# Optimization experiments

Hardware: AMD Instinct MI355X
Metric: run time of the kernel (lower is better)

The kernel has to match this reference:

```python
import jax, jax.numpy as jnp
import numpy as np
from jax import lax

B, D, DEPTH, H, P, NP, IMG, PS = 16, 384, 6, 6, 2000, 4, 224, 16
N = (IMG // PS) ** 2  # 196 patches
T = N + 1             # +cls token
TEMP = 100.0
NEG = -100000.0


def layernorm(x, s, b, eps=1e-6):
    m = jnp.mean(x, -1, keepdims=True)
    v = jnp.var(x, -1, keepdims=True)
    return (x - m) * lax.rsqrt(v + eps) * s + b


def setup_inputs() -> dict:
    key = jax.random.key(0)
    ks = jax.random.split(key, 16)
    s = 0.02
    inp = {
        "x": jax.random.normal(ks[0], (B, 3, IMG, IMG), jnp.float32),
        "patch_w": jax.random.normal(ks[1], (D, 3, PS, PS), jnp.float32) * s,
        "patch_b": jnp.zeros((D,), jnp.float32),
        "cls_token": jax.random.normal(ks[2], (1, 1, D), jnp.float32) * s,
        "pos_embed": jax.random.normal(ks[3], (1, T, D), jnp.float32) * s,
        "ln1_s": jnp.ones((DEPTH, D), jnp.float32),
        "ln1_b": jnp.zeros((DEPTH, D), jnp.float32),
        "qkv_w": jax.random.normal(ks[4], (DEPTH, D, 3 * D), jnp.float32) * s,
        "qkv_b": jnp.zeros((DEPTH, 3 * D), jnp.float32),
        "proj_w": jax.random.normal(ks[5], (DEPTH, D, D), jnp.float32) * s,
        "proj_b": jnp.zeros((DEPTH, D), jnp.float32),
        "ln2_s": jnp.ones((DEPTH, D), jnp.float32),
        "ln2_b": jnp.zeros((DEPTH, D), jnp.float32),
        "fc1_w": jax.random.normal(ks[6], (DEPTH, D, 4 * D), jnp.float32) * s,
        "fc1_b": jnp.zeros((DEPTH, 4 * D), jnp.float32),
        "fc2_w": jax.random.normal(ks[7], (DEPTH, 4 * D, D), jnp.float32) * s,
        "fc2_b": jnp.zeros((DEPTH, D), jnp.float32),
        "norm_s": jnp.ones((D,), jnp.float32),
        "norm_b": jnp.zeros((D,), jnp.float32),
        "proto": jax.random.normal(ks[8], (P, D, NP), jnp.float32),
        "patch_select": jnp.full((1, P, NP), 0.1, jnp.float32),
    }
    return inp


def vit_features(x, patch_w, patch_b, cls_token, pos_embed, blk, norm_s, norm_b):
    # patch embed: non-overlapping 16x16 conv, NCHW/OIHW
    f = lax.conv_general_dilated(x, patch_w, (PS, PS), "VALID",
                                 dimension_numbers=("NCHW", "OIHW", "NCHW"))
    f = f + patch_b[None, :, None, None]              # (B, D, 14, 14)
    tok = f.reshape(B, D, N).transpose(0, 2, 1)        # (B, N, D)
    tok = jnp.concatenate([jnp.broadcast_to(cls_token, (B, 1, D)), tok], axis=1)
    tok = tok + pos_embed

    hd = D // H
    scale = hd ** -0.5

    def block(t, p):
        l1s, l1b, qw, qb, pw, pb, l2s, l2b, f1w, f1b, f2w, f2b = p
        h = layernorm(t, l1s, l1b)
        qkv = h @ qw + qb                              # (B, T, 3D)
        q, k, v = jnp.split(qkv, 3, axis=-1)
        q = q.reshape(B, T, H, hd).transpose(0, 2, 1, 3)
        k = k.reshape(B, T, H, hd).transpose(0, 2, 1, 3)
        v = v.reshape(B, T, H, hd).transpose(0, 2, 1, 3)
        att = jax.nn.softmax(jnp.einsum("bhqd,bhkd->bhqk", q, k) * scale, axis=-1)
        o = jnp.einsum("bhqk,bhkd->bhqd", att, v).transpose(0, 2, 1, 3).reshape(B, T, D)
        t = t + (o @ pw + pb)
        h = layernorm(t, l2s, l2b)
        t = t + (jax.nn.gelu(h @ f1w + f1b, approximate=False) @ f2w + f2b)
        return t, None

    tok, _ = lax.scan(block, tok, blk)
    tok = layernorm(tok, norm_s, norm_b)
    cls = tok[:, 0]                                    # (B, D)
    x_focal = tok[:, 1:] - cls[:, None, :]             # (B, N, D)
    feat = x_focal.transpose(0, 2, 1)                  # (B, D, N) == (B,D,14,14) flat
    return feat, cls


def reference(x, patch_w, patch_b, cls_token, pos_embed, ln1_s, ln1_b, qkv_w,
              qkv_b, proj_w, proj_b, ln2_s, ln2_b, fc1_w, fc1_b, fc2_w, fc2_b,
              norm_s, norm_b, proto, patch_select):
    blk = (ln1_s, ln1_b, qkv_w, qkv_b, proj_w, proj_b, ln2_s, ln2_b,
           fc1_w, fc1_b, fc2_w, fc2_b)
    feat, cls = vit_features(x, patch_w, patch_b, cls_token, pos_embed, blk,
                             norm_s, norm_b)
    # L2-normalize over channel dim (torch F.normalize, eps=1e-12)
    fn = feat / jnp.maximum(jnp.linalg.norm(feat, axis=1, keepdims=True), 1e-12)
    pn = proto / jnp.maximum(jnp.linalg.norm(proto, axis=1, keepdims=True), 1e-12)
    # cosine sims for every (prototype, patch, subpatch): (B, P, N, NP)
    dist = jnp.einsum("bdn,pdk->bpnk", fn, pn).reshape(B, P, N * NP)

    slots = jax.nn.sigmoid(patch_select * TEMP)        # (1, P, NP)
    factor = slots.sum(-1, keepdims=True) + 1e-10

    mask = jnp.ones((B, P, N * NP), dist.dtype)
    col = jnp.arange(N * NP)
    vals = []
    for _ in range(NP):  # greedy non-overlapping subpatch matching
        dm = dist + (1.0 - mask) * NEG
        ids = jnp.argmax(dm, axis=-1)                  # (B, P)
        vals.append(jnp.take_along_axis(dm, ids[..., None], axis=-1)[..., 0])
        mask = jnp.where(col[None, None, :] == ids[..., None], 0.0, mask)
    values = jnp.stack(vals, axis=-1)                  # (B, P, NP)
    proto_scores = (values * (slots * NP / factor)).sum(-1)  # (B, P)
    return cls, proto_scores
```

## Files before the change

### kernel.cpp

```cpp
#include <hip/hip_runtime.h>
#include <hip/hip_bf16.h>
#include <math.h>


#define MROWS 3152

typedef short bf16x8 __attribute__((ext_vector_type(8)));
typedef float f32x4 __attribute__((ext_vector_type(4)));
typedef unsigned short u16;

__device__ __forceinline__ void async_copy16(void* lds, const void* g) {
    __builtin_amdgcn_global_load_lds((const __attribute__((address_space(1))) unsigned int*)g,
                                     (__attribute__((address_space(3))) unsigned int*)lds,
                                     16, 0, 0);
}

__device__ __forceinline__ u16 f2b(float x) {
    __hip_bfloat16 h = __float2bfloat16(x);
    return *(u16*)&h;
}

__global__ void k_cvt(const float* __restrict__ in, __hip_bfloat16* __restrict__ o, int n) {
    int i = blockIdx.x * 256 + threadIdx.x;
    if (i < n) o[i] = __float2bfloat16(in[i]);
}

__global__ __launch_bounds__(256) void k_wt(const float* __restrict__ W, __hip_bfloat16* __restrict__ Wt,
                                            int K, int N) {
    __shared__ float t[32][33];
    const float* src = W + (size_t)blockIdx.z * K * N;
    __hip_bfloat16* dst = Wt + (size_t)blockIdx.z * K * N;
    int n0 = blockIdx.x * 32, k0 = blockIdx.y * 32;
    int tx = threadIdx.x & 31, ty = threadIdx.x >> 5;
    #pragma unroll
    for (int i = 0; i < 4; ++i) t[ty + i * 8][tx] = src[(size_t)(k0 + ty + i * 8) * N + n0 + tx];
    __syncthreads();
    #pragma unroll
    for (int i = 0; i < 4; ++i)
        dst[(size_t)(n0 + ty + i * 8) * K + k0 + tx] = __float2bfloat16(t[tx][ty + i * 8]);
}

__global__ void k_im2col(const float* __restrict__ x, __hip_bfloat16* __restrict__ Acol) {
    int idx = blockIdx.x * 256 + threadIdx.x;
    int k = idx % 768;
    int m = idx / 768;
    int b = m / 196, n = m % 196;
    int c = k >> 8, rem = k & 255, i = rem >> 4, j = rem & 15;
    int py = n / 14, px = n % 14;
    Acol[idx] = __float2bfloat16(x[((b * 3 + c) * 224 + py * 16 + i) * 224 + px * 16 + j]);
}

template<int RES, int GELU, int BF16OUT>
__global__ __launch_bounds__(256) void k_mfma_gemm(
    const u16* __restrict__ A, const u16* __restrict__ Bt,
    const float* __restrict__ bias, const float* __restrict__ res,
    float* __restrict__ Cf, __hip_bfloat16* __restrict__ Cb,
    int M, int N, int K)
{
    __shared__ u16 As[2][128 * 64];
    __shared__ u16 Bs[2][128 * 64];
    const int tid = threadIdx.x;
    const int wid = tid >> 6, lane = tid & 63;
    const int m0 = blockIdx.y * 128, n0 = blockIdx.x * 128;
    const int srow = tid >> 3;
    const int selem = (tid & 7) << 3;
    const int wm = (wid >> 1) * 64, wn = (wid & 1) * 64;

    f32x4 acc[4][4] = {};

    auto stage = [&](int buf, int kb) {
        #pragma unroll
        for (int g = 0; g < 4; ++g) {
            int r = g * 32 + srow;
            int sw = selem ^ ((r & 7) << 3);
            int gr = m0 + r; if (gr > M - 1) gr = M - 1;
            async_copy16(&As[buf][r * 64 + selem], A + (size_t)gr * K + kb + sw);
            async_copy16(&Bs[buf][r * 64 + selem], Bt + (size_t)(n0 + r) * K + kb + sw);
        }
    };

    const int nk = K >> 6;
    stage(0, 0);
    __syncthreads();
    for (int t = 0; t < nk; ++t) {
        const int cur = t & 1;
        if (t + 1 < nk) stage(cur ^ 1, (t + 1) << 6);
        #pragma unroll
        for (int ks = 0; ks < 64; ks += 32) {
            const int kk = ks + ((lane >> 4) << 3);
            bf16x8 af[4], bfr[4];
            #pragma unroll
            for (int i = 0; i < 4; ++i) {
                int r = wm + i * 16 + (lane & 15);
                af[i] = *(const bf16x8*)&As[cur][r * 64 + (kk ^ ((r & 7) << 3))];
            }
            #pragma unroll
            for (int j = 0; j < 4; ++j) {
                int r = wn + j * 16 + (lane & 15);
                bfr[j] = *(const bf16x8*)&Bs[cur][r * 64 + (kk ^ ((r & 7) << 3))];
            }
            #pragma unroll
            for (int i = 0; i < 4; ++i)
                #pragma unroll
                for (int j = 0; j < 4; ++j)
                    acc[i][j] = __builtin_amdgcn_mfma_f32_16x16x32_bf16(af[i], bfr[j], acc[i][j], 0, 0, 0);
        }
        __syncthreads();
    }
    const int cl = lane & 15, rg = (lane >> 4) << 2;
    #pragma unroll
    for (int i = 0; i < 4; ++i) {
        #pragma unroll
        for (int j = 0; j < 4; ++j) {
            const int col = n0 + wn + j * 16 + cl;
            const float bv = bias[col];
            #pragma unroll
            for (int r = 0; r < 4; ++r) {
                const int row = m0 + wm + i * 16 + rg + r;
                if (row >= M) continue;
                float v = acc[i][j][r] + bv;
                if (RES) v += res[(size_t)row * N + col];
                if (GELU) v = 0.5f * v * (1.0f + erff(v * 0.70710678118f));
                if (BF16OUT) Cb[(size_t)row * N + col] = __float2bfloat16(v);
                else         Cf[(size_t)row * N + col] = v;
            }
        }
    }
}

template<int RES, int GELU, int BF16OUT>
__global__ __launch_bounds__(256) void k_mfma_gemm64(
    const u16* __restrict__ A, const u16* __restrict__ Bt,
    const float* __restrict__ bias, const float* __restrict__ res,
    float* __restrict__ Cf, __hip_bfloat16* __restrict__ Cb,
    int M, int N, int K)
{
    __shared__ u16 As[2][128 * 64];
    __shared__ u16 Bs[2][64 * 64];
    const int tid = threadIdx.x;
    const int wid = tid >> 6, lane = tid & 63;
    const int m0 = blockIdx.y * 128, n0 = blockIdx.x * 64;
    const int srow = tid >> 3;
    const int selem = (tid & 7) << 3;
    const int wm = wid * 32;

    f32x4 acc[2][4] = {};

    auto stage = [&](int buf, int kb) {
        #pragma unroll
        for (int g = 0; g < 4; ++g) {
            int r = g * 32 + srow;
            int sw = selem ^ ((r & 7) << 3);
            int gr = m0 + r; if (gr > M - 1) gr = M - 1;
            async_copy16(&As[buf][r * 64 + selem], A + (size_t)gr * K + kb + sw);
        }
        #pragma unroll
        for (int g = 0; g < 2; ++g) {
            int r = g * 32 + srow;
            int sw = selem ^ ((r & 7) << 3);
            async_copy16(&Bs[buf][r * 64 + selem], Bt + (size_t)(n0 + r) * K + kb + sw);
        }
    };

    const int nk = K >> 6;
    stage(0, 0);
    __syncthreads();
    for (int t = 0; t < nk; ++t) {
        const int cur = t & 1;
        if (t + 1 < nk) stage(cur ^ 1, (t + 1) << 6);
        #pragma unroll
        for (int ks = 0; ks < 64; ks += 32) {
            const int kk = ks + ((lane >> 4) << 3);
            bf16x8 af[2], bfr[4];
            #pragma unroll
            for (int i = 0; i < 2; ++i) {
                int r = wm + i * 16 + (lane & 15);
                af[i] = *(const bf16x8*)&As[cur][r * 64 + (kk ^ ((r & 7) << 3))];
            }
            #pragma unroll
            for (int j = 0; j < 4; ++j) {
                int r = j * 16 + (lane & 15);
                bfr[j] = *(const bf16x8*)&Bs[cur][r * 64 + (kk ^ ((r & 7) << 3))];
            }
            #pragma unroll
            for (int i = 0; i < 2; ++i)
                #pragma unroll
                for (int j = 0; j < 4; ++j)
                    acc[i][j] = __builtin_amdgcn_mfma_f32_16x16x32_bf16(af[i], bfr[j], acc[i][j], 0, 0, 0);
        }
        __syncthreads();
    }
    const int cl = lane & 15, rg = (lane >> 4) << 2;
    #pragma unroll
    for (int i = 0; i < 2; ++i) {
        #pragma unroll
        for (int j = 0; j < 4; ++j) {
            const int col = n0 + j * 16 + cl;
            const float bv = bias[col];
            #pragma unroll
            for (int r = 0; r < 4; ++r) {
                const int row = m0 + wm + i * 16 + rg + r;
                if (row >= M) continue;
                float v = acc[i][j][r] + bv;
                if (RES) v += res[(size_t)row * N + col];
                if (GELU) v = 0.5f * v * (1.0f + erff(v * 0.70710678118f));
                if (BF16OUT) Cb[(size_t)row * N + col] = __float2bfloat16(v);
                else         Cf[(size_t)row * N + col] = v;
            }
        }
    }
}

__global__ void k_assemble(const float* __restrict__ ptmp, const float* __restrict__ cls_tok,
                           const float* __restrict__ pos, float* __restrict__ tok) {
    int idx = blockIdx.x * 256 + threadIdx.x;
    int d = idx % 384;
    int t = (idx / 384) % 197;
    int b = idx / (384 * 197);
    float v = (t == 0) ? cls_tok[d] : ptmp[((size_t)b * 196 + t - 1) * 384 + d];
    tok[idx] = v + pos[t * 384 + d];
}

template<typename OT>
__global__ __launch_bounds__(256) void k_ln(const float* __restrict__ X, const float* __restrict__ s,
                                            const float* __restrict__ bb, OT* __restrict__ Y, int rows) {
    int wid = threadIdx.x >> 6, lane = threadIdx.x & 63;
    int row = blockIdx.x * 4 + wid;
    if (row >= rows) return;
    const float* x = X + (size_t)row * 384;
    float v[6], sum = 0.f, sq = 0.f;
    #pragma unroll
    for (int i = 0; i < 6; ++i) { float t = x[lane + 64 * i]; v[i] = t; sum += t; sq += t * t; }
    #pragma unroll
    for (int m = 32; m > 0; m >>= 1) { sum += __shfl_xor(sum, m); sq += __shfl_xor(sq, m); }
    float mean = sum * (1.f / 384.f);
    float var  = sq * (1.f / 384.f) - mean * mean;
    float rstd = rsqrtf(var + 1e-6f);
    OT* y = Y + (size_t)row * 384;
    #pragma unroll
    for (int i = 0; i < 6; ++i) {
        int d = lane + 64 * i;
        float o = (v[i] - mean) * rstd * s[d] + bb[d];
        y[d] = (OT)o;
    }
}

__global__ __launch_bounds__(256) void k_attn_mfma(const u16* __restrict__ qkv, u16* __restrict__ o) {
    __shared__ u16 Ks[208 * 64];
    __shared__ u16 VT[64 * 256];
    __shared__ u16 Pl[4][16 * 256];
    const int bh = blockIdx.x;
    const int b = bh / 6, hh = bh % 6;
    const u16* base = qkv + (size_t)b * 197 * 1152 + hh * 64;
    const int tid = threadIdx.x, wid = tid >> 6, lane = tid & 63;

    for (int i = tid; i < 64 * 59; i += 256) {
        int d = i / 59, k = 197 + i % 59;
        VT[d * 256 + (k ^ ((d & 7) << 3))] = 0;
    }
    for (int i = tid; i < 64 * 48; i += 256) {
        int q = i / 48, k = 208 + i % 48;
        Pl[q >> 4][(q & 15) * 256 + (k ^ ((q & 7) << 3))] = 0;
    }
    for (int i = tid; i < 197 * 8; i += 256) {
        int r = i >> 3, cc = (i & 7) << 3;
        uint4 v = *(const uint4*)(base + (size_t)r * 1152 + 384 + cc);
        *(uint4*)&Ks[r * 64 + (cc ^ ((r & 7) << 3))] = v;
    }
    for (int i = tid; i < 197 * 8; i += 256) {
        int r = i >> 3, d0 = (i & 7) << 3;
        uint4 v = *(const uint4*)(base + (size_t)r * 1152 + 768 + d0);
        const u16* pv = (const u16*)&v;
        #pragma unroll
        for (int j = 0; j < 8; ++j) {
            int d = d0 + j;
            VT[d * 256 + (r ^ ((d & 7) << 3))] = pv[j];
        }
    }
    __syncthreads();

    const int g = lane >> 4, c = lane & 15;
    const int t0 = blockIdx.y * 7;
    const int nt = blockIdx.y ? 6 : 7;
    for (int t = wid; t < nt; t += 4) {
        const int qt = t0 + t;
        const int q0 = qt * 16;
        int qrow = q0 + c; if (qrow > 196) qrow = 196;
        bf16x8 aq[2];
        aq[0] = *(const bf16x8*)(base + (size_t)qrow * 1152 + g * 8);
        aq[1] = *(const bf16x8*)(base + (size_t)qrow * 1152 + 32 + g * 8);

        f32x4 acc[13] = {};
        #pragma unroll
        for (int j = 0; j < 13; ++j) {
            int kr = j * 16 + c;
            bf16x8 b0 = *(const bf16x8*)&Ks[kr * 64 + ((g * 8) ^ ((kr & 7) << 3))];
            bf16x8 b1 = *(const bf16x8*)&Ks[kr * 64 + ((32 + g * 8) ^ ((kr & 7) << 3))];
            acc[j] = __builtin_amdgcn_mfma_f32_16x16x32_bf16(aq[0], b0, acc[j], 0, 0, 0);
            acc[j] = __builtin_amdgcn_mfma_f32_16x16x32_bf16(aq[1], b1, acc[j], 0, 0, 0);
        }

        float sc[13][4];
        float mr[4] = {-1e30f, -1e30f, -1e30f, -1e30f};
        #pragma unroll
        for (int j = 0; j < 13; ++j) {
            bool valid = (j * 16 + c) < 197;
            #pragma unroll
            for (int r = 0; r < 4; ++r) {
                float v = valid ? acc[j][r] * 0.125f : -1e30f;
                sc[j][r] = v;
                mr[r] = fmaxf(mr[r], v);
            }
        }
        #pragma unroll
        for (int r = 0; r < 4; ++r) {
            #pragma unroll
            for (int msk = 1; msk <= 8; msk <<= 1) mr[r] = fmaxf(mr[r], __shfl_xor(mr[r], msk));
        }
        float lr[4] = {0.f, 0.f, 0.f, 0.f};
        #pragma unroll
        for (int j = 0; j < 13; ++j)
            #pragma unroll
            for (int r = 0; r < 4; ++r) { float e = __expf(sc[j][r] - mr[r]); sc[j][r] = e; lr[r] += e; }
        #pragma unroll
        for (int r = 0; r < 4; ++r) {
            #pragma unroll
            for (int msk = 1; msk <= 8; msk <<= 1) lr[r] += __shfl_xor(lr[r], msk);
            lr[r] = 1.f / lr[r];
        }
        #pragma unroll
        for (int j = 0; j < 13; ++j) {
            int col = j * 16 + c;
            #pragma unroll
            for (int r = 0; r < 4; ++r) {
                int q = g * 4 + r;
                Pl[wid][q * 256 + (col ^ ((q & 7) << 3))] = f2b(sc[j][r] * lr[r]);
            }
        }
        asm volatile("s_waitcnt lgkmcnt(0)" ::: "memory");

        f32x4 av[4] = {};
        #pragma unroll
        for (int ks = 0; ks < 7; ++ks) {
            int kk = ks * 32 + g * 8;
            bf16x8 ap = *(const bf16x8*)&Pl[wid][c * 256 + (kk ^ ((c & 7) << 3))];
            #pragma unroll
            for (int jd = 0; jd < 4; ++jd) {
                int dr = jd * 16 + c;
                bf16x8 bv = *(const bf16x8*)&VT[dr * 256 + (kk ^ ((dr & 7) << 3))];
                av[jd] = __builtin_amdgcn_mfma_f32_16x16x32_bf16(ap, bv, av[jd], 0, 0, 0);
            }
        }
        #pragma unroll
        for (int jd = 0; jd < 4; ++jd) {
            #pragma unroll
            for (int r = 0; r < 4; ++r) {
                int q = q0 + g * 4 + r;
                if (q < 197)
                    o[((size_t)b * 197 + q) * 384 + hh * 64 + jd * 16 + c] = f2b(av[jd][r]);
            }
        }
    }
}

__global__ __launch_bounds__(256) void k_fn(const float* __restrict__ tokn, __hip_bfloat16* __restrict__ fn,
                                            float* __restrict__ out) {
    int wid = threadIdx.x >> 6, lane = threadIdx.x & 63;
    int row = blockIdx.x * 4 + wid;
    int b = row / 196, n = row % 196;
    const float* xr = tokn + ((size_t)b * 197 + 1 + n) * 384;
    const float* cr = tokn + (size_t)b * 197 * 384;
    float v[6], ss = 0.f;
    #pragma unroll
    for (int i = 0; i < 6; ++i) {
        int d = lane + 64 * i;
        float t = xr[d] - cr[d];
        v[i] = t; ss += t * t;
    }
    #pragma unroll
    for (int m = 32; m > 0; m >>= 1) ss += __shfl_xor(ss, m);
    float inv = 1.f / fmaxf(sqrtf(ss), 1e-12f);
    #pragma unroll
    for (int i = 0; i < 6; ++i) fn[(size_t)row * 384 + lane + 64 * i] = __float2bfloat16(v[i] * inv);
    int idx = blockIdx.x * 256 + threadIdx.x;
    if (idx < 6144) out[idx] = tokn[(size_t)(idx / 384) * 197 * 384 + idx % 384];
}

__global__ __launch_bounds__(256) void k_pn(const float* __restrict__ proto, __hip_bfloat16* __restrict__ pn) {
    int p = blockIdx.x;
    int k = threadIdx.x >> 6, lane = threadIdx.x & 63;
    float v[6], ss = 0.f;
    #pragma unroll
    for (int i = 0; i < 6; ++i) {
        int d = lane + 64 * i;
        float t = proto[((size_t)p * 384 + d) * 4 + k];
        v[i] = t; ss += t * t;
    }
    #pragma unroll
    for (int m = 32; m > 0; m >>= 1) ss += __shfl_xor(ss, m);
    float inv = 1.f / fmaxf(sqrtf(ss), 1e-12f);
    #pragma unroll
    for (int i = 0; i < 6; ++i) pn[((size_t)p * 4 + k) * 384 + lane + 64 * i] = __float2bfloat16(v[i] * inv);
}

__device__ __forceinline__ void top4_insert(float v, float& t0, float& t1, float& t2, float& t3) {
    if (v > t3) {
        t3 = v;
        if (t3 > t2) { float t = t2; t2 = t3; t3 = t; }
        if (t2 > t1) { float t = t1; t1 = t2; t2 = t; }
        if (t1 > t0) { float t = t0; t0 = t1; t1 = t; }
    }
}

__global__ __launch_bounds__(256) void k_dist_mfma(
    const __hip_bfloat16* __restrict__ fnb, const __hip_bfloat16* __restrict__ pnb,
    const float* __restrict__ psel, float* __restrict__ out)
{
    __shared__ u16 Ap[128 * 64];
    __shared__ u16 Bf[208 * 64];
    const u16* fn = (const u16*)fnb;
    const u16* pn = (const u16*)pnb;
    const int b = blockIdx.x;
    const int pb = blockIdx.y;
    const int tid = threadIdx.x, wid = tid >> 6, lane = tid & 63;
    const int srow = tid >> 3;
    const int selem = (tid & 7) << 3;

    f32x4 acc[2][13] = {};

    for (int kt = 0; kt < 384; kt += 64) {
        __syncthreads();
        #pragma unroll
        for (int g = 0; g < 4; ++g) {
            int r = g * 32 + srow;
            int gr = pb * 128 + r; if (gr > 7999) gr = 7999;
            async_copy16(&Ap[r * 64 + selem],
                         pn + (size_t)gr * 384 + kt + (selem ^ ((r & 7) << 3)));
        }
        #pragma unroll
        for (int g = 0; g < 7; ++g) {
            int r = g * 32 + srow;
            if (r < 208) {
                int fr = r > 195 ? 195 : r;
                async_copy16(&Bf[r * 64 + selem],
                             fn + ((size_t)b * 196 + fr) * 384 + kt + (selem ^ ((r & 7) << 3)));
            }
        }
        __syncthreads();
        #pragma unroll
        for (int ks = 0; ks < 64; ks += 32) {
            const int kk = ks + ((lane >> 4) << 3);
            bf16x8 af[2];
            #pragma unroll
            for (int i = 0; i < 2; ++i) {
                int r = wid * 32 + i * 16 + (lane & 15);
                af[i] = *(const bf16x8*)&Ap[r * 64 + (kk ^ ((r & 7) << 3))];
            }
            #pragma unroll
            for (int j = 0; j < 13; ++j) {
                int r = j * 16 + (lane & 15);
                bf16x8 bj = *(const bf16x8*)&Bf[r * 64 + (kk ^ ((r & 7) << 3))];
                acc[0][j] = __builtin_amdgcn_mfma_f32_16x16x32_bf16(af[0], bj, acc[0][j], 0, 0, 0);
                acc[1][j] = __builtin_amdgcn_mfma_f32_16x16x32_bf16(af[1], bj, acc[1][j], 0, 0, 0);
            }
        }
    }
    const int cl = lane & 15;
    #pragma unroll
    for (int mi = 0; mi < 2; ++mi) {
        float t0 = -1e30f, t1 = -1e30f, t2 = -1e30f, t3 = -1e30f;
        #pragma unroll
        for (int j = 0; j < 13; ++j) {
            if (j * 16 + cl >= 196) continue;
            #pragma unroll
            for (int r = 0; r < 4; ++r) top4_insert(acc[mi][j][r], t0, t1, t2, t3);
        }
        #pragma unroll
        for (int m = 1; m <= 8; m <<= 1) {
            float u0 = __shfl_xor(t0, m), u1 = __shfl_xor(t1, m);
            float u2 = __shfl_xor(t2, m), u3 = __shfl_xor(t3, m);
            top4_insert(u0, t0, t1, t2, t3);
            top4_insert(u1, t0, t1, t2, t3);
            top4_insert(u2, t0, t1, t2, t3);
            top4_insert(u3, t0, t1, t2, t3);
        }
        if (cl == 0) {
            int proto = pb * 32 + wid * 8 + mi * 4 + (lane >> 4);
            if (proto < 2000) {
                float sl[4], fac = 1e-10f;
                #pragma unroll
                for (int i = 0; i < 4; ++i) {
                    sl[i] = 1.f / (1.f + expf(-psel[proto * 4 + i] * 100.f));
                    fac += sl[i];
                }
                float score = (t0 * sl[0] + t1 * sl[1] + t2 * sl[2] + t3 * sl[3]) * 4.f / fac;
                out[6144 + (size_t)b * 2000 + proto] = score;
            }
        }
    }
}

extern "C" void kernel_launch(void* const* d_in, const int* in_sizes, int n_in,
                              void* d_out, int out_size, void* d_ws, size_t ws_size,
                              hipStream_t stream) {
    const float* x       = (const float*)d_in[0];
    const float* patch_w = (const float*)d_in[1];
    const float* patch_b = (const float*)d_in[2];
    const float* cls_tok = (const float*)d_in[3];
    const float* pos     = (const float*)d_in[4];
    const float* ln1_s   = (const float*)d_in[5];
    const float* ln1_b   = (const float*)d_in[6];
    const float* qkv_w   = (const float*)d_in[7];
    const float* qkv_b   = (const float*)d_in[8];
    const float* proj_w  = (const float*)d_in[9];
    const float* proj_b  = (const float*)d_in[10];
    const float* ln2_s   = (const float*)d_in[11];
    const float* ln2_b   = (const float*)d_in[12];
    const float* fc1_w   = (const float*)d_in[13];
    const float* fc1_b   = (const float*)d_in[14];
    const float* fc2_w   = (const float*)d_in[15];
    const float* fc2_b   = (const float*)d_in[16];
    const float* norm_s  = (const float*)d_in[17];
    const float* norm_b  = (const float*)d_in[18];
    const float* proto   = (const float*)d_in[19];
    const float* psel    = (const float*)d_in[20];
    float* out = (float*)d_out;
    char* w = (char*)d_ws;

    __hip_bfloat16* wPb  = (__hip_bfloat16*)(w);
    __hip_bfloat16* wQ   = (__hip_bfloat16*)(w + 589824);
    __hip_bfloat16* wPr  = (__hip_bfloat16*)(w + 5898240);
    __hip_bfloat16* wF1  = (__hip_bfloat16*)(w + 7667712);
    __hip_bfloat16* wF2  = (__hip_bfloat16*)(w + 14745600);
    __hip_bfloat16* Acol = (__hip_bfloat16*)(w + 21823488);
    float*          ptmp = (float*)         (w + 26640384);
    float*          tok  = (float*)         (w + 31457280);
    __hip_bfloat16* hbf  = (__hip_bfloat16*)(w + 36298752);
    __hip_bfloat16* qkvb = (__hip_bfloat16*)(w + 38719488);
    __hip_bfloat16* aob  = (__hip_bfloat16*)(w + 53243904);
    __hip_bfloat16* hbig = (__hip_bfloat16*)(w + 55664640);
    float*          hf   = (float*)         (w + 65347584);
    __hip_bfloat16* fnb  = (__hip_bfloat16*)(w + 70189056);
    __hip_bfloat16* pnb  = (__hip_bfloat16*)(w + 72597504);

    k_cvt<<<1152, 256, 0, stream>>>(patch_w, wPb, 294912);
    k_wt<<<dim3(36, 12, 6), 256, 0, stream>>>(qkv_w, wQ, 384, 1152);
    k_wt<<<dim3(12, 12, 6), 256, 0, stream>>>(proj_w, wPr, 384, 384);
    k_wt<<<dim3(48, 12, 6), 256, 0, stream>>>(fc1_w, wF1, 384, 1536);
    k_wt<<<dim3(12, 48, 6), 256, 0, stream>>>(fc2_w, wF2, 1536, 384);

    k_im2col<<<9408, 256, 0, stream>>>(x, Acol);
    k_mfma_gemm64<0,0,0><<<dim3(6, 25), 256, 0, stream>>>(
        (const u16*)Acol, (const u16*)wPb, patch_b, nullptr, ptmp, nullptr, 3136, 384, 768);
    k_assemble<<<4728, 256, 0, stream>>>(ptmp, cls_tok, pos, tok);

    for (int l = 0; l < 6; ++l) {
        k_ln<__hip_bfloat16><<<788, 256, 0, stream>>>(tok, ln1_s + l * 384, ln1_b + l * 384, hbf, MROWS);
        k_mfma_gemm<0,0,1><<<dim3(9, 25), 256, 0, stream>>>(
            (const u16*)hbf, (const u16*)(wQ + (size_t)l * 1152 * 384), qkv_b + l * 1152,
            nullptr, nullptr, qkvb, MROWS, 1152, 384);
        k_attn_mfma<<<dim3(96, 2), 256, 0, stream>>>((const u16*)qkvb, (u16*)aob);
        k_mfma_gemm64<1,0,0><<<dim3(6, 25), 256, 0, stream>>>(
            (const u16*)aob, (const u16*)(wPr + (size_t)l * 384 * 384), proj_b + l * 384,
            tok, tok, nullptr, MROWS, 384, 384);
        k_ln<__hip_bfloat16><<<788, 256, 0, stream>>>(tok, ln2_s + l * 384, ln2_b + l * 384, hbf, MROWS);
        k_mfma_gemm<0,1,1><<<dim3(12, 25), 256, 0, stream>>>(
            (const u16*)hbf, (const u16*)(wF1 + (size_t)l * 1536 * 384), fc1_b + l * 1536,
            nullptr, nullptr, hbig, MROWS, 1536, 384);
        k_mfma_gemm64<1,0,0><<<dim3(6, 25), 256, 0, stream>>>(
            (const u16*)hbig, (const u16*)(wF2 + (size_t)l * 384 * 1536), fc2_b + l * 384,
            tok, tok, nullptr, MROWS, 384, 1536);
    }

    k_ln<float><<<788, 256, 0, stream>>>(tok, norm_s, norm_b, hf, MROWS);
    k_fn<<<784, 256, 0, stream>>>(hf, fnb, out);
    k_pn<<<2000, 256, 0, stream>>>(proto, pnb);
    k_dist_mfma<<<dim3(16, 63), 256, 0, stream>>>(fnb, pnb, psel, out);
}
```

Baseline: 685.6 us.

## Fuse transformer layers into one cooperative persistent megakernel with grid syncs

Replaces the per-layer sequence of separate kernel launches (LN, QKV GEMM, attention, proj GEMM, LN, FC1, FC2) with one cooperative kernel of 256 blocks that loops over phases separated by grid-wide syncs. It also fuses patch-embed bias and positional add directly into the token buffer, moves cls-token init into the weight-convert kernel, and fuses the final LN with normalization. This removes about 40 launch gaps and intermediate buffers. In exchange, occupancy is fixed at 256 blocks with 64KB of shared memory each, some phases use fewer tiles than blocks, and every grid sync costs time.

New measurement: 1.903 ms. 2.78x slower.

```diff
diff --git a/kernel.cpp b/kernel.cpp
--- a/kernel.cpp
+++ b/kernel.cpp
@@ -1,9 +1,13 @@
 #include <hip/hip_runtime.h>
 #include <hip/hip_bf16.h>
+#include <hip/hip_cooperative_groups.h>
 #include <math.h>
 
+namespace cg = cooperative_groups;
+
 
 #define MROWS 3152
+#define SMEM_BYTES 65536
 
 typedef short bf16x8 __attribute__((ext_vector_type(8)));
 typedef float f32x4 __attribute__((ext_vector_type(4)));
@@ -20,9 +24,15 @@
     return *(u16*)&h;
 }
 
-__global__ void k_cvt(const float* __restrict__ in, __hip_bfloat16* __restrict__ o, int n) {
+__global__ void k_cvt(const float* __restrict__ in, __hip_bfloat16* __restrict__ o, int n,
+                      const float* __restrict__ cls_tok, const float* __restrict__ pos,
+                      float* __restrict__ tok) {
     int i = blockIdx.x * 256 + threadIdx.x;
     if (i < n) o[i] = __float2bfloat16(in[i]);
+    if (i < 6144) {
+        int b = i / 384, d = i % 384;
+        tok[(size_t)b * 197 * 384 + d] = cls_tok[d] + pos[d];
+    }
 }
 
 __global__ __launch_bounds__(256) void k_wt(const float* __restrict__ W, __hip_bfloat16* __restrict__ Wt,
@@ -50,91 +60,12 @@
     Acol[idx] = __float2bfloat16(x[((b * 3 + c) * 224 + py * 16 + i) * 224 + px * 16 + j]);
 }
 
-template<int RES, int GELU, int BF16OUT>
-__global__ __launch_bounds__(256) void k_mfma_gemm(
+__global__ __launch_bounds__(256) void k_patch_tok(
     const u16* __restrict__ A, const u16* __restrict__ Bt,
-    const float* __restrict__ bias, const float* __restrict__ res,
-    float* __restrict__ Cf, __hip_bfloat16* __restrict__ Cb,
-    int M, int N, int K)
+    const float* __restrict__ bias, const float* __restrict__ pos,
+    float* __restrict__ tok)
 {
-    __shared__ u16 As[2][128 * 64];
-    __shared__ u16 Bs[2][128 * 64];
-    const int tid = threadIdx.x;
-    const int wid = tid >> 6, lane = tid & 63;
-    const int m0 = blockIdx.y * 128, n0 = blockIdx.x * 128;
-    const int srow = tid >> 3;
-    const int selem = (tid & 7) << 3;
-    const int wm = (wid >> 1) * 64, wn = (wid & 1) * 64;
-
-    f32x4 acc[4][4] = {};
-
-    auto stage = [&](int buf, int kb) {
-        #pragma unroll
-        for (int g = 0; g < 4; ++g) {
-            int r = g * 32 + srow;
-            int sw = selem ^ ((r & 7) << 3);
-            int gr = m0 + r; if (gr > M - 1) gr = M - 1;
-            async_copy16(&As[buf][r * 64 + selem], A + (size_t)gr * K + kb + sw);
-            async_copy16(&Bs[buf][r * 64 + selem], Bt + (size_t)(n0 + r) * K + kb + sw);
-        }
-    };
-
-    const int nk = K >> 6;
-    stage(0, 0);
-    __syncthreads();
-    for (int t = 0; t < nk; ++t) {
-        const int cur = t & 1;
-        if (t + 1 < nk) stage(cur ^ 1, (t + 1) << 6);
-        #pragma unroll
-        for (int ks = 0; ks < 64; ks += 32) {
-            const int kk = ks + ((lane >> 4) << 3);
-            bf16x8 af[4], bfr[4];
-            #pragma unroll
-            for (int i = 0; i < 4; ++i) {
-                int r = wm + i * 16 + (lane & 15);
-                af[i] = *(const bf16x8*)&As[cur][r * 64 + (kk ^ ((r & 7) << 3))];
-            }
-            #pragma unroll
-            for (int j = 0; j < 4; ++j) {
-                int r = wn + j * 16 + (lane & 15);
-                bfr[j] = *(const bf16x8*)&Bs[cur][r * 64 + (kk ^ ((r & 7) << 3))];
-            }
-            #pragma unroll
-            for (int i = 0; i < 4; ++i)
-                #pragma unroll
-                for (int j = 0; j < 4; ++j)
-                    acc[i][j] = __builtin_amdgcn_mfma_f32_16x16x32_bf16(af[i], bfr[j], acc[i][j], 0, 0, 0);
-        }
-        __syncthreads();
-    }
-    const int cl = lane & 15, rg = (lane >> 4) << 2;
-    #pragma unroll
-    for (int i = 0; i < 4; ++i) {
-        #pragma unroll
-        for (int j = 0; j < 4; ++j) {
-            const int col = n0 + wn + j * 16 + cl;
-            const float bv = bias[col];
-            #pragma unroll
-            for (int r = 0; r < 4; ++r) {
-                const int row = m0 + wm + i * 16 + rg + r;
-                if (row >= M) continue;
-                float v = acc[i][j][r] + bv;
-                if (RES) v += res[(size_t)row * N + col];
-                if (GELU) v = 0.5f * v * (1.0f + erff(v * 0.70710678118f));
-                if (BF16OUT) Cb[(size_t)row * N + col] = __float2bfloat16(v);
-                else         Cf[(size_t)row * N + col] = v;
-            }
-        }
-    }
-}
-
-template<int RES, int GELU, int BF16OUT>
-__global__ __launch_bounds__(256) void k_mfma_gemm64(
-    const u16* __restrict__ A, const u16* __restrict__ Bt,
-    const float* __restrict__ bias, const float* __restrict__ res,
-    float* __restrict__ Cf, __hip_bfloat16* __restrict__ Cb,
-    int M, int N, int K)
-{
+    const int M = 3136, K = 768;
     __shared__ u16 As[2][128 * 64];
     __shared__ u16 Bs[2][64 * 64];
     const int tid = threadIdx.x;
@@ -201,66 +132,209 @@
             for (int r = 0; r < 4; ++r) {
                 const int row = m0 + wm + i * 16 + rg + r;
                 if (row >= M) continue;
-                float v = acc[i][j][r] + bv;
-                if (RES) v += res[(size_t)row * N + col];
-                if (GELU) v = 0.5f * v * (1.0f + erff(v * 0.70710678118f));
-                if (BF16OUT) Cb[(size_t)row * N + col] = __float2bfloat16(v);
-                else         Cf[(size_t)row * N + col] = v;
-            }
-        }
-    }
-}
-
-__global__ void k_assemble(const float* __restrict__ ptmp, const float* __restrict__ cls_tok,
-                           const float* __restrict__ pos, float* __restrict__ tok) {
-    int idx = blockIdx.x * 256 + threadIdx.x;
-    int d = idx % 384;
-    int t = (idx / 384) % 197;
-    int b = idx / (384 * 197);
-    float v = (t == 0) ? cls_tok[d] : ptmp[((size_t)b * 196 + t - 1) * 384 + d];
-    tok[idx] = v + pos[t * 384 + d];
-}
-
-template<typename OT>
-__global__ __launch_bounds__(256) void k_ln(const float* __restrict__ X, const float* __restrict__ s,
-                                            const float* __restrict__ bb, OT* __restrict__ Y, int rows) {
-    int wid = threadIdx.x >> 6, lane = threadIdx.x & 63;
-    int row = blockIdx.x * 4 + wid;
-    if (row >= rows) return;
-    const float* x = X + (size_t)row * 384;
-    float v[6], sum = 0.f, sq = 0.f;
-    #pragma unroll
-    for (int i = 0; i < 6; ++i) { float t = x[lane + 64 * i]; v[i] = t; sum += t; sq += t * t; }
-    #pragma unroll
-    for (int m = 32; m > 0; m >>= 1) { sum += __shfl_xor(sum, m); sq += __shfl_xor(sq, m); }
-    float mean = sum * (1.f / 384.f);
-    float var  = sq * (1.f / 384.f) - mean * mean;
-    float rstd = rsqrtf(var + 1e-6f);
-    OT* y = Y + (size_t)row * 384;
-    #pragma unroll
-    for (int i = 0; i < 6; ++i) {
-        int d = lane + 64 * i;
-        float o = (v[i] - mean) * rstd * s[d] + bb[d];
-        y[d] = (OT)o;
-    }
-}
-
-__global__ __launch_bounds__(256) void k_attn_mfma(const u16* __restrict__ qkv, u16* __restrict__ o) {
-    __shared__ u16 Ks[208 * 64];
-    __shared__ u16 VT[64 * 256];
-    __shared__ u16 Pl[4][16 * 256];
-    const int bh = blockIdx.x;
+                int b = row / 196, n = row % 196;
+                float v = acc[i][j][r] + bv + pos[(size_t)(1 + n) * 384 + col];
+                tok[((size_t)b * 197 + 1 + n) * 384 + col] = v;
+            }
+        }
+    }
+}
+
+
+__device__ __forceinline__ void ln_phase(const float* __restrict__ X, const float* __restrict__ s,
+                                         const float* __restrict__ bb, u16* __restrict__ Y,
+                                         int bid, int tid) {
+    int wid = tid >> 6, lane = tid & 63;
+    for (int u = bid; u < 788; u += 256) {
+        int row = u * 4 + wid;
+        const float* x = X + (size_t)row * 384;
+        float v[6], sum = 0.f, sq = 0.f;
+        #pragma unroll
+        for (int i = 0; i < 6; ++i) { float t = x[lane + 64 * i]; v[i] = t; sum += t; sq += t * t; }
+        #pragma unroll
+        for (int m = 32; m > 0; m >>= 1) { sum += __shfl_xor(sum, m); sq += __shfl_xor(sq, m); }
+        float mean = sum * (1.f / 384.f);
+        float var  = sq * (1.f / 384.f) - mean * mean;
+        float rstd = rsqrtf(var + 1e-6f);
+        u16* y = Y + (size_t)row * 384;
+        #pragma unroll
+        for (int i = 0; i < 6; ++i) {
+            int d = lane + 64 * i;
+            y[d] = f2b((v[i] - mean) * rstd * s[d] + bb[d]);
+        }
+    }
+}
+
+__device__ __forceinline__ void gemm128_phase(
+    const u16* __restrict__ A, const u16* __restrict__ Bt,
+    const float* __restrict__ bias, u16* __restrict__ Cb,
+    int M, int N, int K, int nb, int ntiles, int gelu,
+    char* smem, int bid, int tid)
+{
+    u16* As = (u16*)smem;
+    u16* Bs = (u16*)(smem + 32768);
+    const int wid = tid >> 6, lane = tid & 63;
+    const int srow = tid >> 3;
+    const int selem = (tid & 7) << 3;
+    const int wm = (wid >> 1) * 64, wn = (wid & 1) * 64;
+
+    for (int t = bid; t < ntiles; t += 256) {
+        const int m0 = (t / nb) * 128, n0 = (t % nb) * 128;
+        f32x4 acc[4][4] = {};
+
+        auto stage = [&](int buf, int kb) {
+            #pragma unroll
+            for (int g = 0; g < 4; ++g) {
+                int r = g * 32 + srow;
+                int sw = selem ^ ((r & 7) << 3);
+                int gr = m0 + r; if (gr > M - 1) gr = M - 1;
+                async_copy16(&As[buf * 8192 + r * 64 + selem], A + (size_t)gr * K + kb + sw);
+                async_copy16(&Bs[buf * 8192 + r * 64 + selem], Bt + (size_t)(n0 + r) * K + kb + sw);
+            }
+        };
+
+        const int nk = K >> 6;
+        stage(0, 0);
+        __syncthreads();
+        for (int kt = 0; kt < nk; ++kt) {
+            const int cur = kt & 1;
+            if (kt + 1 < nk) stage(cur ^ 1, (kt + 1) << 6);
+            #pragma unroll
+            for (int ks = 0; ks < 64; ks += 32) {
+                const int kk = ks + ((lane >> 4) << 3);
+                bf16x8 af[4], bfr[4];
+                #pragma unroll
+                for (int i = 0; i < 4; ++i) {
+                    int r = wm + i * 16 + (lane & 15);
+                    af[i] = *(const bf16x8*)&As[cur * 8192 + r * 64 + (kk ^ ((r & 7) << 3))];
+                }
+                #pragma unroll
+                for (int j = 0; j < 4; ++j) {
+                    int r = wn + j * 16 + (lane & 15);
+                    bfr[j] = *(const bf16x8*)&Bs[cur * 8192 + r * 64 + (kk ^ ((r & 7) << 3))];
+                }
+                #pragma unroll
+                for (int i = 0; i < 4; ++i)
+                    #pragma unroll
+                    for (int j = 0; j < 4; ++j)
+                        acc[i][j] = __builtin_amdgcn_mfma_f32_16x16x32_bf16(af[i], bfr[j], acc[i][j], 0, 0, 0);
+            }
+            __syncthreads();
+        }
+        const int cl = lane & 15, rg = (lane >> 4) << 2;
+        #pragma unroll
+        for (int i = 0; i < 4; ++i) {
+            #pragma unroll
+            for (int j = 0; j < 4; ++j) {
+                const int col = n0 + wn + j * 16 + cl;
+                const float bv = bias[col];
+                #pragma unroll
+                for (int r = 0; r < 4; ++r) {
+                    const int row = m0 + wm + i * 16 + rg + r;
+                    if (row >= M) continue;
+                    float v = acc[i][j][r] + bv;
+                    if (gelu) v = 0.5f * v * (1.0f + erff(v * 0.70710678118f));
+                    Cb[(size_t)row * N + col] = f2b(v);
+                }
+            }
+        }
+    }
+}
+
+__device__ __forceinline__ void gemm64_res_phase(
+    const u16* __restrict__ A, const u16* __restrict__ Bt,
+    const float* __restrict__ bias, float* __restrict__ tok,
+    int M, int K, int ntiles, char* smem, int bid, int tid)
+{
+    const int N = 384;
+    u16* As = (u16*)smem;
+    u16* Bs = (u16*)(smem + 32768);
+    const int wid = tid >> 6, lane = tid & 63;
+    const int srow = tid >> 3;
+    const int selem = (tid & 7) << 3;
+    const int wm = wid * 32;
+
+    for (int t = bid; t < ntiles; t += 256) {
+        const int m0 = (t / 6) * 128, n0 = (t % 6) * 64;
+        f32x4 acc[2][4] = {};
+
+        auto stage = [&](int buf, int kb) {
+            #pragma unroll
+            for (int g = 0; g < 4; ++g) {
+                int r = g * 32 + srow;
+                int sw = selem ^ ((r & 7) << 3);
+                int gr = m0 + r; if (gr > M - 1) gr = M - 1;
+                async_copy16(&As[buf * 8192 + r * 64 + selem], A + (size_t)gr * K + kb + sw);
+            }
+            #pragma unroll
+            for (int g = 0; g < 2; ++g) {
+                int r = g * 32 + srow;
+                int sw = selem ^ ((r & 7) << 3);
+                async_copy16(&Bs[buf * 4096 + r * 64 + selem], Bt + (size_t)(n0 + r) * K + kb + sw);
+            }
+        };
+
+        const int nk = K >> 6;
+        stage(0, 0);
+        __syncthreads();
+        for (int kt = 0; kt < nk; ++kt) {
+            const int cur = kt & 1;
+            if (kt + 1 < nk) stage(cur ^ 1, (kt + 1) << 6);
+            #pragma unroll
+            for (int ks = 0; ks < 64; ks += 32) {
+                const int kk = ks + ((lane >> 4) << 3);
+                bf16x8 af[2], bfr[4];
+                #pragma unroll
+                for (int i = 0; i < 2; ++i) {
+                    int r = wm + i * 16 + (lane & 15);
+                    af[i] = *(const bf16x8*)&As[cur * 8192 + r * 64 + (kk ^ ((r & 7) << 3))];
+                }
+                #pragma unroll
+                for (int j = 0; j < 4; ++j) {
+                    int r = j * 16 + (lane & 15);
+                    bfr[j] = *(const bf16x8*)&Bs[cur * 4096 + r * 64 + (kk ^ ((r & 7) << 3))];
+                }
+                #pragma unroll
+                for (int i = 0; i < 2; ++i)
+                    #pragma unroll
+                    for (int j = 0; j < 4; ++j)
+                        acc[i][j] = __builtin_amdgcn_mfma_f32_16x16x32_bf16(af[i], bfr[j], acc[i][j], 0, 0, 0);
+            }
+            __syncthreads();
+        }
+        const int cl = lane & 15, rg = (lane >> 4) << 2;
+        #pragma unroll
+        for (int i = 0; i < 2; ++i) {
+            #pragma unroll
+            for (int j = 0; j < 4; ++j) {
+                const int col = n0 + j * 16 + cl;
+                const float bv = bias[col];
+                #pragma unroll
+                for (int r = 0; r < 4; ++r) {
+                    const int row = m0 + wm + i * 16 + rg + r;
+                    if (row >= M) continue;
+                    size_t idx = (size_t)row * N + col;
+                    tok[idx] = acc[i][j][r] + bv + tok[idx];
+                }
+            }
+        }
+    }
+}
+
+__device__ __forceinline__ void attn_phase(const u16* __restrict__ qkv, u16* __restrict__ o,
+                                           char* smem, int bid, int tid) {
+    if (bid >= 192) return;
+    u16* Ks = (u16*)smem;
+    u16* VT = (u16*)(smem + 26624);
+    u16* Pl = (u16*)(smem + 59392);
+    const int bh = bid >> 1, yhalf = bid & 1;
     const int b = bh / 6, hh = bh % 6;
     const u16* base = qkv + (size_t)b * 197 * 1152 + hh * 64;
-    const int tid = threadIdx.x, wid = tid >> 6, lane = tid & 63;
+    const int wid = tid >> 6, lane = tid & 63;
 
     for (int i = tid; i < 64 * 59; i += 256) {
         int d = i / 59, k = 197 + i % 59;
         VT[d * 256 + (k ^ ((d & 7) << 3))] = 0;
-    }
-    for (int i = tid; i < 64 * 48; i += 256) {
-        int q = i / 48, k = 208 + i % 48;
-        Pl[q >> 4][(q & 15) * 256 + (k ^ ((q & 7) << 3))] = 0;
     }
     for (int i = tid; i < 197 * 8; i += 256) {
         int r = i >> 3, cc = (i & 7) << 3;
@@ -280,11 +354,11 @@
     __syncthreads();
 
     const int g = lane >> 4, c = lane & 15;
-    const int t0 = blockIdx.y * 7;
-    const int nt = blockIdx.y ? 6 : 7;
+    u16* Pw = Pl + wid * 512;
+    const int t0 = yhalf * 7;
+    const int nt = yhalf ? 6 : 7;
     for (int t = wid; t < nt; t += 4) {
-        const int qt = t0 + t;
-        const int q0 = qt * 16;
+        const int q0 = (t0 + t) * 16;
         int qrow = q0 + c; if (qrow > 196) qrow = 196;
         bf16x8 aq[2];
         aq[0] = *(const bf16x8*)(base + (size_t)qrow * 1152 + g * 8);
@@ -328,22 +402,23 @@
             for (int msk = 1; msk <= 8; msk <<= 1) lr[r] += __shfl_xor(lr[r], msk);
             lr[r] = 1.f / lr[r];
         }
-        #pragma unroll
-        for (int j = 0; j < 13; ++j) {
-            int col = j * 16 + c;
-            #pragma unroll
-            for (int r = 0; r < 4; ++r) {
-                int q = g * 4 + r;
-                Pl[wid][q * 256 + (col ^ ((q & 7) << 3))] = f2b(sc[j][r] * lr[r]);
-            }
-        }
-        asm volatile("s_waitcnt lgkmcnt(0)" ::: "memory");
 
         f32x4 av[4] = {};
-        #pragma unroll
-        for (int ks = 0; ks < 7; ++ks) {
-            int kk = ks * 32 + g * 8;
-            bf16x8 ap = *(const bf16x8*)&Pl[wid][c * 256 + (kk ^ ((c & 7) << 3))];
+        for (int ch = 0; ch < 7; ++ch) {
+            #pragma unroll
+            for (int jj = 0; jj < 2; ++jj) {
+                int j = ch * 2 + jj;
+                int blk = (jj << 1) + (c >> 3);
+                #pragma unroll
+                for (int r = 0; r < 4; ++r) {
+                    int q = g * 4 + r;
+                    float val = (j < 13) ? sc[j][r] * lr[r] : 0.f;
+                    Pw[q * 32 + ((blk ^ g) << 3) + (c & 7)] = f2b(val);
+                }
+            }
+            asm volatile("s_waitcnt lgkmcnt(0)" ::: "memory");
+            bf16x8 ap = *(const bf16x8*)&Pw[c * 32 + (((g ^ (c >> 2)) & 3) << 3)];
+            const int kk = ch * 32 + g * 8;
             #pragma unroll
             for (int jd = 0; jd < 4; ++jd) {
                 int dr = jd * 16 + c;
@@ -363,27 +438,105 @@
     }
 }
 
-__global__ __launch_bounds__(256) void k_fn(const float* __restrict__ tokn, __hip_bfloat16* __restrict__ fn,
-                                            float* __restrict__ out) {
-    int wid = threadIdx.x >> 6, lane = threadIdx.x & 63;
-    int row = blockIdx.x * 4 + wid;
-    int b = row / 196, n = row % 196;
-    const float* xr = tokn + ((size_t)b * 197 + 1 + n) * 384;
-    const float* cr = tokn + (size_t)b * 197 * 384;
-    float v[6], ss = 0.f;
+__device__ __forceinline__ void lnvals(const float* __restrict__ x, const float* __restrict__ s,
+                                       const float* __restrict__ bb, int lane, float* v) {
+    float sum = 0.f, sq = 0.f;
+    #pragma unroll
+    for (int i = 0; i < 6; ++i) { float t = x[lane + 64 * i]; v[i] = t; sum += t; sq += t * t; }
+    #pragma unroll
+    for (int m = 32; m > 0; m >>= 1) { sum += __shfl_xor(sum, m); sq += __shfl_xor(sq, m); }
+    float mean = sum * (1.f / 384.f);
+    float var  = sq * (1.f / 384.f) - mean * mean;
+    float rstd = rsqrtf(var + 1e-6f);
     #pragma unroll
     for (int i = 0; i < 6; ++i) {
         int d = lane + 64 * i;
-        float t = xr[d] - cr[d];
-        v[i] = t; ss += t * t;
-    }
-    #pragma unroll
-    for (int m = 32; m > 0; m >>= 1) ss += __shfl_xor(ss, m);
-    float inv = 1.f / fmaxf(sqrtf(ss), 1e-12f);
-    #pragma unroll
-    for (int i = 0; i < 6; ++i) fn[(size_t)row * 384 + lane + 64 * i] = __float2bfloat16(v[i] * inv);
-    int idx = blockIdx.x * 256 + threadIdx.x;
-    if (idx < 6144) out[idx] = tokn[(size_t)(idx / 384) * 197 * 384 + idx % 384];
+        v[i] = (v[i] - mean) * rstd * s[d] + bb[d];
+    }
+}
+
+__device__ __forceinline__ void fnln_phase(const float* __restrict__ tok, const float* __restrict__ s,
+                                           const float* __restrict__ bb, u16* __restrict__ fnb,
+                                           float* __restrict__ out, int bid, int tid) {
+    int wid = tid >> 6, lane = tid & 63;
+    for (int u = bid; u < 788; u += 256) {
+        int row = u * 4 + wid;
+        int b = row / 197, t = row % 197;
+        float v1[6];
+        lnvals(tok + (size_t)row * 384, s, bb, lane, v1);
+        if (t == 0) {
+            #pragma unroll
+            for (int i = 0; i < 6; ++i) out[(size_t)b * 384 + lane + 64 * i] = v1[i];
+        } else {
+            float v0[6];
+            lnvals(tok + (size_t)b * 197 * 384, s, bb, lane, v0);
+            float d[6], ss = 0.f;
+            #pragma unroll
+            for (int i = 0; i < 6; ++i) { d[i] = v1[i] - v0[i]; ss += d[i] * d[i]; }
+            #pragma unroll
+            for (int m = 32; m > 0; m >>= 1) ss += __shfl_xor(ss, m);
+            float inv = 1.f / fmaxf(sqrtf(ss), 1e-12f);
+            #pragma unroll
+            for (int i = 0; i < 6; ++i)
+                fnb[((size_t)b * 196 + t - 1) * 384 + lane + 64 * i] = f2b(d[i] * inv);
+        }
+    }
+}
+
+__global__ __launch_bounds__(256) void k_mega(
+    float* tok, u16* hbf, u16* qkvb, u16* aob, u16* hbig,
+    const u16* wQ, const u16* wPr, const u16* wF1, const u16* wF2,
+    const float* qkv_b, const float* proj_b, const float* fc1_b, const float* fc2_b,
+    const float* ln1_s, const float* ln1_b, const float* ln2_s, const float* ln2_b,
+    const float* norm_s, const float* norm_b, u16* fnb, float* out)
+{
+    cg::grid_group gg = cg::this_grid();
+    __shared__ __align__(16) char smem[SMEM_BYTES];
+    const int bid = blockIdx.x, tid = threadIdx.x;
+
+    for (int l = 0; l < 6; ++l) {
+        ln_phase(tok, ln1_s + l * 384, ln1_b + l * 384, hbf, bid, tid);
+        gg.sync();
+        gemm128_phase(hbf, wQ + (size_t)l * 1152 * 384, qkv_b + l * 1152, qkvb,
+                      MROWS, 1152, 384, 9, 225, 0, smem, bid, tid);
+        gg.sync();
+        attn_phase(qkvb, aob, smem, bid, tid);
+        gg.sync();
+        gemm64_res_phase(aob, wPr + (size_t)l * 384 * 384, proj_b + l * 384, tok,
+                         MROWS, 384, 150, smem, bid, tid);
+        gg.sync();
+        ln_phase(tok, ln2_s + l * 384, ln2_b + l * 384, hbf, bid, tid);
+        gg.sync();
+        gemm128_phase(hbf, wF1 + (size_t)l * 384 * 1536, fc1_b + l * 1536, hbig,
+                      MROWS, 1536, 384, 12, 300, 1, smem, bid, tid);
+        gg.sync();
+        gemm64_res_phase(hbig, wF2 + (size_t)l * 1536 * 384, fc2_b + l * 384, tok,
+                         MROWS, 1536, 150, smem, bid, tid);
+        gg.sync();
+    }
+    fnln_phase(tok, norm_s, norm_b, fnb, out, bid, tid);
+}
+
+__global__ __launch_bounds__(256) void w_ln(const float* X, const float* s, const float* bb, u16* Y) {
+    ln_phase(X, s, bb, Y, blockIdx.x, threadIdx.x);
+}
+__global__ __launch_bounds__(256) void w_gemm128(const u16* A, const u16* Bt, const float* bias, u16* Cb,
+                                                 int M, int N, int K, int nb, int ntiles, int gelu) {
+    __shared__ __align__(16) char smem[SMEM_BYTES];
+    gemm128_phase(A, Bt, bias, Cb, M, N, K, nb, ntiles, gelu, smem, blockIdx.x, threadIdx.x);
+}
+__global__ __launch_bounds__(256) void w_gemm64res(const u16* A, const u16* Bt, const float* bias,
+                                                   float* tok, int M, int K, int ntiles) {
+    __shared__ __align__(16) char smem[SMEM_BYTES];
+    gemm64_res_phase(A, Bt, bias, tok, M, K, ntiles, smem, blockIdx.x, threadIdx.x);
+}
+__global__ __launch_bounds__(256) void w_attn(const u16* qkv, u16* o) {
+    __shared__ __align__(16) char smem[SMEM_BYTES];
+    attn_phase(qkv, o, smem, blockIdx.x, threadIdx.x);
+}
+__global__ __launch_bounds__(256) void w_fnln(const float* tok, const float* s, const float* bb,
+                                              u16* fnb, float* out) {
+    fnln_phase(tok, s, bb, fnb, out, blockIdx.x, threadIdx.x);
 }
 
 __global__ __launch_bounds__(256) void k_pn(const float* __restrict__ proto, __hip_bfloat16* __restrict__ pn) {
@@ -528,52 +681,53 @@
     char* w = (char*)d_ws;
 
     __hip_bfloat16* wPb  = (__hip_bfloat16*)(w);
-    __hip_bfloat16* wQ   = (__hip_bfloat16*)(w + 589824);
-    __hip_bfloat16* wPr  = (__hip_bfloat16*)(w + 5898240);
-    __hip_bfloat16* wF1  = (__hip_bfloat16*)(w + 7667712);
-    __hip_bfloat16* wF2  = (__hip_bfloat16*)(w + 14745600);
+    u16*            wQ   = (u16*)(w + 589824);
+    u16*            wPr  = (u16*)(w + 5898240);
+    u16*            wF1  = (u16*)(w + 7667712);
+    u16*            wF2  = (u16*)(w + 14745600);
     __hip_bfloat16* Acol = (__hip_bfloat16*)(w + 21823488);
-    float*          ptmp = (float*)         (w + 26640384);
     float*          tok  = (float*)         (w + 31457280);
-    __hip_bfloat16* hbf  = (__hip_bfloat16*)(w + 36298752);
-    __hip_bfloat16* qkvb = (__hip_bfloat16*)(w + 38719488);
-    __hip_bfloat16* aob  = (__hip_bfloat16*)(w + 53243904);
-    __hip_bfloat16* hbig = (__hip_bfloat16*)(w + 55664640);
-    float*          hf   = (float*)         (w + 65347584);
-    __hip_bfloat16* fnb  = (__hip_bfloat16*)(w + 70189056);
+    u16*            hbf  = (u16*)(w + 36298752);
+    u16*            qkvb = (u16*)(w + 38719488);
+    u16*            aob  = (u16*)(w + 53243904);
+    u16*            hbig = (u16*)(w + 55664640);
+    u16*            fnb  = (u16*)(w + 70189056);
     __hip_bfloat16* pnb  = (__hip_bfloat16*)(w + 72597504);
 
-    k_cvt<<<1152, 256, 0, stream>>>(patch_w, wPb, 294912);
-    k_wt<<<dim3(36, 12, 6), 256, 0, stream>>>(qkv_w, wQ, 384, 1152);
-    k_wt<<<dim3(12, 12, 6), 256, 0, stream>>>(proj_w, wPr, 384, 384);
-    k_wt<<<dim3(48, 12, 6), 256, 0, stream>>>(fc1_w, wF1, 384, 1536);
-    k_wt<<<dim3(12, 48, 6), 256, 0, stream>>>(fc2_w, wF2, 1536, 384);
-
+    k_cvt<<<1152, 256, 0, stream>>>(patch_w, wPb, 294912, cls_tok, pos, tok);
+    k_wt<<<dim3(36, 12, 6), 256, 0, stream>>>(qkv_w, (__hip_bfloat16*)wQ, 384, 1152);
+    k_wt<<<dim3(12, 12, 6), 256, 0, stream>>>(proj_w, (__hip_bfloat16*)wPr, 384, 384);
+    k_wt<<<dim3(48, 12, 6), 256, 0, stream>>>(fc1_w, (__hip_bfloat16*)wF1, 384, 1536);
+    k_wt<<<dim3(12, 48, 6), 256, 0, stream>>>(fc2_w, (__hip_bfloat16*)wF2, 1536, 384);
     k_im2col<<<9408, 256, 0, stream>>>(x, Acol);
-    k_mfma_gemm64<0,0,0><<<dim3(6, 25), 256, 0, stream>>>(
-        (const u16*)Acol, (const u16*)wPb, patch_b, nullptr, ptmp, nullptr, 3136, 384, 768);
-    k_assemble<<<4728, 256, 0, stream>>>(ptmp, cls_tok, pos, tok);
-
-    for (int l = 0; l < 6; ++l) {
-        k_ln<__hip_bfloat16><<<788, 256, 0, stream>>>(tok, ln1_s + l * 384, ln1_b + l * 384, hbf, MROWS);
-        k_mfma_gemm<0,0,1><<<dim3(9, 25), 256, 0, stream>>>(
-            (const u16*)hbf, (const u16*)(wQ + (size_t)l * 1152 * 384), qkv_b + l * 1152,
-            nullptr, nullptr, qkvb, MROWS, 1152, 384);
-        k_attn_mfma<<<dim3(96, 2), 256, 0, stream>>>((const u16*)qkvb, (u16*)aob);
-        k_mfma_gemm64<1,0,0><<<dim3(6, 25), 256, 0, stream>>>(
-            (const u16*)aob, (const u16*)(wPr + (size_t)l * 384 * 384), proj_b + l * 384,
-            tok, tok, nullptr, MROWS, 384, 384);
-        k_ln<__hip_bfloat16><<<788, 256, 0, stream>>>(tok, ln2_s + l * 384, ln2_b + l * 384, hbf, MROWS);
-        k_mfma_gemm<0,1,1><<<dim3(12, 25), 256, 0, stream>>>(
-            (const u16*)hbf, (const u16*)(wF1 + (size_t)l * 1536 * 384), fc1_b + l * 1536,
-            nullptr, nullptr, hbig, MROWS, 1536, 384);
-        k_mfma_gemm64<1,0,0><<<dim3(6, 25), 256, 0, stream>>>(
-            (const u16*)hbig, (const u16*)(wF2 + (size_t)l * 384 * 1536), fc2_b + l * 384,
-            tok, tok, nullptr, MROWS, 384, 1536);
-    }
-
-    k_ln<float><<<788, 256, 0, stream>>>(tok, norm_s, norm_b, hf, MROWS);
-    k_fn<<<784, 256, 0, stream>>>(hf, fnb, out);
+    k_patch_tok<<<dim3(6, 25), 256, 0, stream>>>((const u16*)Acol, (const u16*)wPb, patch_b, pos, tok);
+
+    void* margs[] = {
+        (void*)&tok, (void*)&hbf, (void*)&qkvb, (void*)&aob, (void*)&hbig,
+        (void*)&wQ, (void*)&wPr, (void*)&wF1, (void*)&wF2,
+        (void*)&qkv_b, (void*)&proj_b, (void*)&fc1_b, (void*)&fc2_b,
+        (void*)&ln1_s, (void*)&ln1_b, (void*)&ln2_s, (void*)&ln2_b,
+        (void*)&norm_s, (void*)&norm_b, (void*)&fnb, (void*)&out
+    };
+    hipError_t cerr = hipLaunchCooperativeKernel((const void*)k_mega, dim3(256), dim3(256),
+                                                 margs, 0, stream);
+    if (cerr != hipSuccess) {
+        for (int l = 0; l < 6; ++l) {
+            w_ln<<<256, 256, 0, stream>>>(tok, ln1_s + l * 384, ln1_b + l * 384, hbf);
+            w_gemm128<<<256, 256, 0, stream>>>(hbf, wQ + (size_t)l * 1152 * 384, qkv_b + l * 1152,
+                                               qkvb, MROWS, 1152, 384, 9, 225, 0);
+            w_attn<<<256, 256, 0, stream>>>(qkvb, aob);
+            w_gemm64res<<<256, 256, 0, stream>>>(aob, wPr + (size_t)l * 384 * 384, proj_b + l * 384,
+                                                 tok, MROWS, 384, 150);
+            w_ln<<<256, 256, 0, stream>>>(tok, ln2_s + l * 384, ln2_b + l * 384, hbf);
+            w_gemm128<<<256, 256, 0, stream>>>(hbf, wF1 + (size_t)l * 384 * 1536, fc1_b + l * 1536,
+                                               hbig, MROWS, 1536, 384, 12, 300, 1);
+            w_gemm64res<<<256, 256, 0, stream>>>(hbig, wF2 + (size_t)l * 1536 * 384, fc2_b + l * 384,
+                                                 tok, MROWS, 1536, 150);
+        }
+        w_fnln<<<256, 256, 0, stream>>>(tok, norm_s, norm_b, fnb, out);
+    }
+
     k_pn<<<2000, 256, 0, stream>>>(proto, pnb);
-    k_dist_mfma<<<dim3(16, 63), 256, 0, stream>>>(fnb, pnb, psel, out);
-}
+    k_dist_mfma<<<dim3(16, 63), 256, 0, stream>>>((const __hip_bfloat16*)fnb, pnb, psel, out);
+}
```
